# Kernel optimization log

Measured on AMD Instinct MI355X. Metric: run time of the kernel, lower is better.

Reference implementation:

```python
import jax, jax.numpy as jnp
import numpy as np
from jax import lax

VOL = 96 ** 3        # AvgPool3d(kernel_size=96) pooling volume
GAMMA = 0.2          # cam_threshold (gamma default in update())
NUM_CLASSES = 14


def conv3d_same(x, w, b):
    # Conv3d(kernel_size=3, padding=1), NCDHW layout
    y = lax.conv_general_dilated(
        x, w, window_strides=(1, 1, 1),
        padding=((1, 1), (1, 1), (1, 1)),
        dimension_numbers=('NCDHW', 'OIDHW', 'NCDHW'))
    return y + b[None, :, None, None, None]


def maxpool3d_2(x):
    return lax.reduce_window(x, -jnp.inf, lax.max,
                             (1, 1, 2, 2, 2), (1, 1, 2, 2, 2), 'VALID')


def dom_classifier(x, c1w, c1b, c2w, c2b, lw, lb):
    x = jax.nn.relu(maxpool3d_2(conv3d_same(x, c1w, c1b)))   # [N,128,2,2,2]
    x = jax.nn.relu(maxpool3d_2(conv3d_same(x, c2w, c2b)))   # [N,64,1,1,1]
    x = x.reshape(x.shape[0], -1)                            # [N,64]
    return x @ lw.T + lb                                     # [N,1]


def get_cam(feature):
    # torch.autograd.functional.jacobian of AvgPool3d(96) on a [1,C,96,96,96]
    # input is analytically delta(c,c')/96^3 at every voxel; the subsequent
    # mean over spatial dims keeps eye(C)/96^3. Same math, closed form.
    n, c = feature.shape[:2]
    weight = jnp.broadcast_to(jnp.eye(c, dtype=feature.dtype) / VOL, (n, c, c))
    # einsum(weight, feature, 'n cls ch, n ch h w d -> n cls h w d')
    cam = jnp.einsum('nkc,ncxyz->nkxyz', weight, feature)
    return jax.nn.relu(cam)


def reference(feature, masks, dom_feat, conv1_w, conv1_b, conv2_w, conv2_b,
              lin_w, lin_b):
    cam = get_cam(feature)[:, 1:]                 # drop background class
    cam = cam * (cam > GAMMA)                     # cam *= cam > threshold
    pseudo = jnp.argmax(cam, axis=1, keepdims=True).astype(masks.dtype)
    updated_masks = masks + pseudo * (masks == 0)
    dom_logits = dom_classifier(dom_feat, conv1_w, conv1_b,
                                conv2_w, conv2_b, lin_w, lin_b)
    return cam, pseudo, updated_masks, dom_logits


def setup_inputs() -> dict:
    key = jax.random.key(0)
    ks = jax.random.split(key, 8)
    return {
        'feature': jax.random.normal(ks[0], (2, NUM_CLASSES, 96, 96, 96), jnp.float32),
        'masks': jax.random.randint(ks[1], (2, 1, 96, 96, 96), 0, NUM_CLASSES, jnp.int32),
        'dom_feat': jax.random.normal(ks[2], (2, 256, 4, 4, 4), jnp.float32),
        'conv1_w': jax.random.normal(ks[3], (128, 256, 3, 3, 3), jnp.float32) * 0.05,
        'conv1_b': jnp.zeros((128,), jnp.float32),
        'conv2_w': jax.random.normal(ks[4], (64, 128, 3, 3, 3), jnp.float32) * 0.05,
        'conv2_b': jnp.zeros((64,), jnp.float32),
        'lin_w': jax.random.normal(ks[5], (1, 64), jnp.float32) * 0.05,
        'lin_b': jnp.zeros((1,), jnp.float32),
    }
```

## Files before the change

### kernel.cpp

```cpp
#include <hip/hip_runtime.h>

#define VOXELS   884736
#define OUT_CAM  0
#define OUT_PSE  23003136
#define OUT_MSK  24772608
#define OUT_LOG  26542080

#define WS_WT 0
#define WS_P  884736
#define WS_H1 1769472

__global__ __launch_bounds__(256) void k_cam(const float* __restrict__ feat,
                                             const int*   __restrict__ masks,
                                             float* __restrict__ out) {
  int bx = blockIdx.x;
  int n  = bx >= 864;
  int q  = (bx - n * 864) * 256 + threadIdx.x;
  int v  = q * 4;
  const float scale = 1.0f / 884736.0f;

  float4 best;
  int4 bi = {0, 0, 0, 0};
#pragma unroll
  for (int k = 0; k < 13; ++k) {
    const float4 f = *(const float4*)(feat + (size_t)(n * 14 + 1 + k) * VOXELS + v);
    float4 t;
    t.x = f.x * scale; t.x = (t.x > 0.2f) ? t.x : 0.0f;
    t.y = f.y * scale; t.y = (t.y > 0.2f) ? t.y : 0.0f;
    t.z = f.z * scale; t.z = (t.z > 0.2f) ? t.z : 0.0f;
    t.w = f.w * scale; t.w = (t.w > 0.2f) ? t.w : 0.0f;
    *(float4*)(out + OUT_CAM + (size_t)(n * 13 + k) * VOXELS + v) = t;
    if (k == 0) {
      best = t;
    } else {
      if (t.x > best.x) { best.x = t.x; bi.x = k; }
      if (t.y > best.y) { best.y = t.y; bi.y = k; }
      if (t.z > best.z) { best.z = t.z; bi.z = k; }
      if (t.w > best.w) { best.w = t.w; bi.w = k; }
    }
  }
  const int4 m = *(const int4*)(masks + (size_t)n * VOXELS + v);
  float4 ps = {(float)bi.x, (float)bi.y, (float)bi.z, (float)bi.w};
  float4 um;
  um.x = (m.x == 0) ? ps.x : (float)m.x;
  um.y = (m.y == 0) ? ps.y : (float)m.y;
  um.z = (m.z == 0) ? ps.z : (float)m.z;
  um.w = (m.w == 0) ? ps.w : (float)m.w;
  *(float4*)(out + OUT_PSE + (size_t)n * VOXELS + v) = ps;
  *(float4*)(out + OUT_MSK + (size_t)n * VOXELS + v) = um;
}

__global__ __launch_bounds__(256) void k_wprep(const float* __restrict__ w1,
                                               float* __restrict__ wt) {
  int idx = blockIdx.x * 256 + threadIdx.x;
  int oc = idx & 127;
  int rest = idx >> 7;
  int ic = rest & 255;
  int tap = rest >> 8;
  wt[idx] = w1[(oc * 256 + ic) * 27 + tap];
}

__global__ __launch_bounds__(256) void k_conv1(const float* __restrict__ dom,
                                               const float* __restrict__ wt,
                                               float* __restrict__ P) {
  __shared__ float Wl[128 * 64];
  __shared__ float Xl[128 * 64];
  int bx = blockIdx.x;
  int och = bx & 1;
  int ich = (bx >> 1) & 1;
  int rest = bx >> 2;
  int tap = rest % 27;
  int n = rest / 27;
  int kd = tap / 9 - 1, kh = (tap % 9) / 3 - 1, kw = tap % 3 - 1;
  int I0 = ich * 128, O0 = och * 64;
  int tid = threadIdx.x;

  for (int i = tid; i < 2048; i += 256) {
    int kk = i >> 4, oc4 = (i & 15) << 2;
    *(float4*)&Wl[kk * 64 + oc4] =
        *(const float4*)&wt[(size_t)(tap * 256 + I0 + kk) * 128 + O0 + oc4];
  }
  for (int i = tid; i < 8192; i += 256) {
    int kk = i >> 6, pos = i & 63;
    int d = pos >> 4, h = (pos >> 2) & 3, w = pos & 3;
    int sd = d + kd, sh = h + kh, sw = w + kw;
    bool ok = ((unsigned)sd < 4u) && ((unsigned)sh < 4u) && ((unsigned)sw < 4u);
    Xl[i] = ok ? dom[((n * 256 + I0 + kk) << 6) + sd * 16 + sh * 4 + sw] : 0.0f;
  }
  __syncthreads();

  int to = tid >> 4, tp = tid & 15;
  float4 acc0 = {0, 0, 0, 0}, acc1 = {0, 0, 0, 0}, acc2 = {0, 0, 0, 0}, acc3 = {0, 0, 0, 0};
#pragma unroll 4
  for (int kk = 0; kk < 128; ++kk) {
    float4 a = *(float4*)&Wl[kk * 64 + to * 4];
    float4 b = *(float4*)&Xl[kk * 64 + tp * 4];
    acc0.x += a.x * b.x; acc0.y += a.x * b.y; acc0.z += a.x * b.z; acc0.w += a.x * b.w;
    acc1.x += a.y * b.x; acc1.y += a.y * b.y; acc1.z += a.y * b.z; acc1.w += a.y * b.w;
    acc2.x += a.z * b.x; acc2.y += a.z * b.y; acc2.z += a.z * b.z; acc2.w += a.z * b.w;
    acc3.x += a.w * b.x; acc3.y += a.w * b.y; acc3.z += a.w * b.z; acc3.w += a.w * b.w;
  }
  float* pb = P + (size_t)((tap * 2 + ich) * 2 + n) * 8192 + (O0 + to * 4) * 64 + tp * 4;
  *(float4*)(pb +   0) = acc0;
  *(float4*)(pb +  64) = acc1;
  *(float4*)(pb + 128) = acc2;
  *(float4*)(pb + 192) = acc3;
}

__global__ __launch_bounds__(64) void k_pool1(const float* __restrict__ P,
                                              const float* __restrict__ b1,
                                              float* __restrict__ h1) {
  __shared__ float s[64];
  int n = blockIdx.x >> 7, oc = blockIdx.x & 127;
  int tid = threadIdx.x;
  float sum = b1[oc];
#pragma unroll
  for (int sl = 0; sl < 54; ++sl)
    sum += P[((size_t)(sl * 2 + n) * 128 + oc) * 64 + tid];
  s[tid] = sum;
  __syncthreads();
  if (tid < 8) {
    int pd = tid >> 2, ph = (tid >> 1) & 1, pw = tid & 1;
    float m = -3.402823466e38f;
#pragma unroll
    for (int dd = 0; dd < 2; ++dd)
#pragma unroll
      for (int hh = 0; hh < 2; ++hh)
#pragma unroll
        for (int ww = 0; ww < 2; ++ww)
          m = fmaxf(m, s[(pd * 2 + dd) * 16 + (ph * 2 + hh) * 4 + (pw * 2 + ww)]);
    h1[(n * 128 + oc) * 8 + tid] = fmaxf(m, 0.0f);
  }
}

__global__ __launch_bounds__(64) void k_conv2(const float* __restrict__ h1,
                                              const float* __restrict__ w2,
                                              const float* __restrict__ b2,
                                              const float* __restrict__ lw,
                                              const float* __restrict__ lb,
                                              float* __restrict__ logits) {
  __shared__ float hl[1024];
  __shared__ float wl[3456];
  __shared__ float red[64];
  int n = blockIdx.x >> 6, oc = blockIdx.x & 63;
  int tid = threadIdx.x;
  for (int i = tid; i < 1024; i += 64) hl[i] = h1[n * 1024 + i];
  for (int i = tid; i < 3456; i += 64) wl[i] = w2[oc * 3456 + i];
  __syncthreads();
  int p = tid & 7, g = tid >> 3;
  int d = p >> 2, h = (p >> 1) & 1, w = p & 1;
  float acc = 0.0f;
  for (int ic = g * 16; ic < g * 16 + 16; ++ic) {
#pragma unroll
    for (int a = 0; a < 2; ++a)
#pragma unroll
      for (int b = 0; b < 2; ++b)
#pragma unroll
        for (int c = 0; c < 2; ++c) {
          int tapi = (a - d + 1) * 9 + (b - h + 1) * 3 + (c - w + 1);
          acc += hl[ic * 8 + a * 4 + b * 2 + c] * wl[ic * 27 + tapi];
        }
  }
  red[tid] = acc;
  __syncthreads();
  if (tid == 0) {
    float mx = -3.402823466e38f;
#pragma unroll
    for (int pp = 0; pp < 8; ++pp) {
      float sv = b2[oc];
#pragma unroll
      for (int gg = 0; gg < 8; ++gg) sv += red[gg * 8 + pp];
      mx = fmaxf(mx, sv);
    }
    float h2v = fmaxf(mx, 0.0f);
    atomicAdd(&logits[n], h2v * lw[oc]);
    if (oc == 0) atomicAdd(&logits[n], lb[0]);
  }
}

extern "C" void kernel_launch(void* const* d_in, const int* in_sizes, int n_in,
                              void* d_out, int out_size, void* d_ws, size_t ws_size,
                              hipStream_t stream) {
  const float* feat  = (const float*)d_in[0];
  const int*   masks = (const int*)  d_in[1];
  const float* dom   = (const float*)d_in[2];
  const float* w1    = (const float*)d_in[3];
  const float* b1    = (const float*)d_in[4];
  const float* w2    = (const float*)d_in[5];
  const float* b2    = (const float*)d_in[6];
  const float* lw    = (const float*)d_in[7];
  const float* lb    = (const float*)d_in[8];
  float* out = (float*)d_out;
  float* ws  = (float*)d_ws;
  float* wt  = ws + WS_WT;
  float* P   = ws + WS_P;
  float* h1  = ws + WS_H1;
  float* logits = out + OUT_LOG;

  hipMemsetAsync(logits, 0, 2 * sizeof(float), stream);
  k_wprep<<<3456, 256, 0, stream>>>(w1, wt);
  k_conv1<<<216, 256, 0, stream>>>(dom, wt, P);
  k_pool1<<<256, 64, 0, stream>>>(P, b1, h1);
  k_conv2<<<128, 64, 0, stream>>>(h1, w2, b2, lw, lb, logits);
  k_cam<<<1728, 256, 0, stream>>>(feat, masks, out);
}
```

Measured before the change: 244.0 us.

## Coalesce weight transpose via LDS, fold memset, batch cam loads, nontemporal stores

The weight-prep kernel now reads w1 rows coalesced through shared memory and writes a [tap][oc][ic] layout. conv1 reads that layout with float4 loads and transposes into a padded LDS tile to avoid bank conflicts. The logits memset is folded into the transpose kernel, removing one launch. The cam kernel issues all 13 feature loads up front to raise memory-level parallelism and uses nontemporal stores for its large outputs. This costs more registers in k_cam and a 27KB LDS buffer in k_trans.

```diff
diff --git a/kernel.cpp b/kernel.cpp
--- a/kernel.cpp
+++ b/kernel.cpp
@@ -9,6 +9,9 @@
 #define WS_WT 0
 #define WS_P  884736
 #define WS_H1 1769472
+
+typedef float  f32x4 __attribute__((ext_vector_type(4)));
+typedef int    i32x4 __attribute__((ext_vector_type(4)));
 
 __global__ __launch_bounds__(256) void k_cam(const float* __restrict__ feat,
                                              const int*   __restrict__ masks,
@@ -19,17 +22,22 @@
   int v  = q * 4;
   const float scale = 1.0f / 884736.0f;
 
-  float4 best;
-  int4 bi = {0, 0, 0, 0};
+  f32x4 f[13];
+#pragma unroll
+  for (int k = 0; k < 13; ++k)
+    f[k] = *(const f32x4*)(feat + (size_t)(n * 14 + 1 + k) * VOXELS + v);
+  const i32x4 m = *(const i32x4*)(masks + (size_t)n * VOXELS + v);
+
+  f32x4 best = {0, 0, 0, 0};
+  i32x4 bi = {0, 0, 0, 0};
 #pragma unroll
   for (int k = 0; k < 13; ++k) {
-    const float4 f = *(const float4*)(feat + (size_t)(n * 14 + 1 + k) * VOXELS + v);
-    float4 t;
-    t.x = f.x * scale; t.x = (t.x > 0.2f) ? t.x : 0.0f;
-    t.y = f.y * scale; t.y = (t.y > 0.2f) ? t.y : 0.0f;
-    t.z = f.z * scale; t.z = (t.z > 0.2f) ? t.z : 0.0f;
-    t.w = f.w * scale; t.w = (t.w > 0.2f) ? t.w : 0.0f;
-    *(float4*)(out + OUT_CAM + (size_t)(n * 13 + k) * VOXELS + v) = t;
+    f32x4 t = f[k] * scale;
+    t.x = (t.x > 0.2f) ? t.x : 0.0f;
+    t.y = (t.y > 0.2f) ? t.y : 0.0f;
+    t.z = (t.z > 0.2f) ? t.z : 0.0f;
+    t.w = (t.w > 0.2f) ? t.w : 0.0f;
+    __builtin_nontemporal_store(t, (f32x4*)(out + OUT_CAM + (size_t)(n * 13 + k) * VOXELS + v));
     if (k == 0) {
       best = t;
     } else {
@@ -39,31 +47,35 @@
       if (t.w > best.w) { best.w = t.w; bi.w = k; }
     }
   }
-  const int4 m = *(const int4*)(masks + (size_t)n * VOXELS + v);
-  float4 ps = {(float)bi.x, (float)bi.y, (float)bi.z, (float)bi.w};
-  float4 um;
+  f32x4 ps = {(float)bi.x, (float)bi.y, (float)bi.z, (float)bi.w};
+  f32x4 um;
   um.x = (m.x == 0) ? ps.x : (float)m.x;
   um.y = (m.y == 0) ? ps.y : (float)m.y;
   um.z = (m.z == 0) ? ps.z : (float)m.z;
   um.w = (m.w == 0) ? ps.w : (float)m.w;
-  *(float4*)(out + OUT_PSE + (size_t)n * VOXELS + v) = ps;
-  *(float4*)(out + OUT_MSK + (size_t)n * VOXELS + v) = um;
-}
-
-__global__ __launch_bounds__(256) void k_wprep(const float* __restrict__ w1,
-                                               float* __restrict__ wt) {
-  int idx = blockIdx.x * 256 + threadIdx.x;
-  int oc = idx & 127;
-  int rest = idx >> 7;
-  int ic = rest & 255;
-  int tap = rest >> 8;
-  wt[idx] = w1[(oc * 256 + ic) * 27 + tap];
-}
-
+  __builtin_nontemporal_store(ps, (f32x4*)(out + OUT_PSE + (size_t)n * VOXELS + v));
+  __builtin_nontemporal_store(um, (f32x4*)(out + OUT_MSK + (size_t)n * VOXELS + v));
+}
+
+__global__ __launch_bounds__(256) void k_trans(const float* __restrict__ w1,
+                                               float* __restrict__ wt,
+                                               float* __restrict__ logits) {
+  __shared__ float s[6912];
+  int r0 = blockIdx.x * 256;
+  int tid = threadIdx.x;
+  if (blockIdx.x == 0 && tid < 2) logits[tid] = 0.0f;
+  for (int i = tid; i < 6912; i += 256) s[i] = w1[(size_t)r0 * 27 + i];
+  __syncthreads();
+#pragma unroll
+  for (int tap = 0; tap < 27; ++tap)
+    wt[tap * 32768 + r0 + tid] = s[tid * 27 + tap];
+}
+
+#define WSTRIDE 68
 __global__ __launch_bounds__(256) void k_conv1(const float* __restrict__ dom,
                                                const float* __restrict__ wt,
                                                float* __restrict__ P) {
-  __shared__ float Wl[128 * 64];
+  __shared__ float Wl[128 * WSTRIDE];
   __shared__ float Xl[128 * 64];
   int bx = blockIdx.x;
   int och = bx & 1;
@@ -76,9 +88,12 @@
   int tid = threadIdx.x;
 
   for (int i = tid; i < 2048; i += 256) {
-    int kk = i >> 4, oc4 = (i & 15) << 2;
-    *(float4*)&Wl[kk * 64 + oc4] =
-        *(const float4*)&wt[(size_t)(tap * 256 + I0 + kk) * 128 + O0 + oc4];
+    int oc = i >> 5, k4 = (i & 31) << 2;
+    f32x4 rd = *(const f32x4*)&wt[(size_t)(tap * 128 + O0 + oc) * 256 + I0 + k4];
+    Wl[(k4 + 0) * WSTRIDE + oc] = rd.x;
+    Wl[(k4 + 1) * WSTRIDE + oc] = rd.y;
+    Wl[(k4 + 2) * WSTRIDE + oc] = rd.z;
+    Wl[(k4 + 3) * WSTRIDE + oc] = rd.w;
   }
   for (int i = tid; i < 8192; i += 256) {
     int kk = i >> 6, pos = i & 63;
@@ -90,21 +105,21 @@
   __syncthreads();
 
   int to = tid >> 4, tp = tid & 15;
-  float4 acc0 = {0, 0, 0, 0}, acc1 = {0, 0, 0, 0}, acc2 = {0, 0, 0, 0}, acc3 = {0, 0, 0, 0};
+  f32x4 acc0 = {0, 0, 0, 0}, acc1 = {0, 0, 0, 0}, acc2 = {0, 0, 0, 0}, acc3 = {0, 0, 0, 0};
 #pragma unroll 4
   for (int kk = 0; kk < 128; ++kk) {
-    float4 a = *(float4*)&Wl[kk * 64 + to * 4];
-    float4 b = *(float4*)&Xl[kk * 64 + tp * 4];
-    acc0.x += a.x * b.x; acc0.y += a.x * b.y; acc0.z += a.x * b.z; acc0.w += a.x * b.w;
-    acc1.x += a.y * b.x; acc1.y += a.y * b.y; acc1.z += a.y * b.z; acc1.w += a.y * b.w;
-    acc2.x += a.z * b.x; acc2.y += a.z * b.y; acc2.z += a.z * b.z; acc2.w += a.z * b.w;
-    acc3.x += a.w * b.x; acc3.y += a.w * b.y; acc3.z += a.w * b.z; acc3.w += a.w * b.w;
+    f32x4 a = *(f32x4*)&Wl[kk * WSTRIDE + to * 4];
+    f32x4 b = *(f32x4*)&Xl[kk * 64 + tp * 4];
+    acc0 += a.x * b;
+    acc1 += a.y * b;
+    acc2 += a.z * b;
+    acc3 += a.w * b;
   }
   float* pb = P + (size_t)((tap * 2 + ich) * 2 + n) * 8192 + (O0 + to * 4) * 64 + tp * 4;
-  *(float4*)(pb +   0) = acc0;
-  *(float4*)(pb +  64) = acc1;
-  *(float4*)(pb + 128) = acc2;
-  *(float4*)(pb + 192) = acc3;
+  *(f32x4*)(pb +   0) = acc0;
+  *(f32x4*)(pb +  64) = acc1;
+  *(f32x4*)(pb + 128) = acc2;
+  *(f32x4*)(pb + 192) = acc3;
 }
 
 __global__ __launch_bounds__(64) void k_pool1(const float* __restrict__ P,
@@ -197,8 +212,7 @@
   float* h1  = ws + WS_H1;
   float* logits = out + OUT_LOG;
 
-  hipMemsetAsync(logits, 0, 2 * sizeof(float), stream);
-  k_wprep<<<3456, 256, 0, stream>>>(w1, wt);
+  k_trans<<<128, 256, 0, stream>>>(w1, wt, logits);
   k_conv1<<<216, 256, 0, stream>>>(dom, wt, P);
   k_pool1<<<256, 64, 0, stream>>>(P, b1, h1);
   k_conv2<<<128, 64, 0, stream>>>(h1, w2, b2, lw, lb, logits);
```

After: 243.0 us. No clear change (-0.4%).
